# Performance work log

Hardware: AMD Instinct MI355X
Metric: run time of the kernel (lower is better)

The kernel has to match this reference:

```python
import jax, jax.numpy as jnp
import numpy as np

B, T, C, H = 8, 1024, 1024, 16
NEG = -1000000000.0
EPS = 1e-12


def setup_inputs() -> dict:
    key = jax.random.key(0)
    ks = jax.random.split(key, 12)
    s = 0.02  # keep pre-softmax logits in a sane range
    return {
        "x": jax.random.normal(ks[0], (B, T, C), jnp.float32),
        "mask": jax.random.randint(ks[1], (B, T), 0, 2, jnp.int32),
        "Wq": jax.random.normal(ks[2], (C, C), jnp.float32) * s,
        "bq": jax.random.normal(ks[3], (C,), jnp.float32) * s,
        "Wk": jax.random.normal(ks[4], (C, C), jnp.float32) * s,
        "bk": jax.random.normal(ks[5], (C,), jnp.float32) * s,
        "Wv": jax.random.normal(ks[6], (C, C), jnp.float32) * s,
        "bv": jax.random.normal(ks[7], (C,), jnp.float32) * s,
        "Wp": jax.random.normal(ks[8], (C, C), jnp.float32) * s,
        "bp": jax.random.normal(ks[9], (C,), jnp.float32) * s,
        "ln_w": jnp.ones((C,), jnp.float32),
        "ln_b": jnp.zeros((C,), jnp.float32),
    }


def reference(x, mask, Wq, bq, Wk, bk, Wv, bv, Wp, bp, ln_w, ln_b):
    Bx, Tx, Cx = x.shape
    hd = Cx // H
    # torch nn.Linear: y = x @ W.T + b
    def lin(inp, W, b):
        return inp @ W.T + b

    def split_heads(t):  # [B,T,C] -> [B,H,T,hd]
        return t.reshape(Bx, Tx, H, hd).transpose(0, 2, 1, 3)

    q = split_heads(lin(x, Wq, bq))
    k = split_heads(lin(x, Wk, bk))
    v = split_heads(lin(x, Wv, bv))

    att = jnp.einsum("bhqd,bhkd->bhqk", q, k) * (1.0 / jnp.sqrt(jnp.float32(hd)))
    # mask [B,T] masks key positions; broadcast to [B,1,1,T]
    att = jnp.where(mask[:, None, None, :] == 0, NEG, att)
    # stable softmax (manual max-subtract, matching original)
    att = jax.nn.softmax(att, axis=-1)
    # dropout prob 0.0 -> identity (eval-mode faithful)
    y = jnp.einsum("bhqk,bhkd->bhqd", att, v)
    y = y.transpose(0, 2, 1, 3).reshape(Bx, Tx, Cx)
    y = lin(y, Wp, bp)
    # residual + LayerNorm(eps=1e-12)
    z = y + x
    mu = jnp.mean(z, axis=-1, keepdims=True)
    var = jnp.mean(jnp.square(z - mu), axis=-1, keepdims=True)
    out = (z - mu) * jax.lax.rsqrt(var + EPS) * ln_w + ln_b
    return out
```

## Files before the change

kernel.cpp:

```cpp
#include <hip/hip_runtime.h>
#include <stdint.h>

#define B_ 8
#define T_ 1024
#define C_ 1024
#define H_ 16
#define HD 64
#define M_TOT (B_ * T_)

using f32x4 = __attribute__((ext_vector_type(4))) float;
using s16x8 = __attribute__((ext_vector_type(8))) short;
using i32x4 = __attribute__((ext_vector_type(4))) int;

__device__ __forceinline__ unsigned short f2bf(float f) {
  unsigned int u = __builtin_bit_cast(unsigned int, f);
  unsigned int r = (u + 0x7fffu + ((u >> 16) & 1u)) >> 16;
  return (unsigned short)r;
}

__device__ __forceinline__ void gload_lds16(const void* g, void* l) {
  __builtin_amdgcn_global_load_lds(
      (const __attribute__((address_space(1))) unsigned int*)g,
      (__attribute__((address_space(3))) unsigned int*)l, 16, 0, 0);
}

__global__ __launch_bounds__(256) void k_convert(
    const float* __restrict__ x, const float* __restrict__ wq,
    const float* __restrict__ wk, const float* __restrict__ wv,
    const float* __restrict__ wp, const float* __restrict__ bq,
    const float* __restrict__ bk, const float* __restrict__ bv,
    const int* __restrict__ maskp, unsigned short* __restrict__ xb,
    unsigned short* __restrict__ wqkv, unsigned short* __restrict__ wpb,
    float* __restrict__ bias_cat, unsigned int* __restrict__ mpair) {
  const long n_x = (long)M_TOT * C_;
  const long W_ELT = (long)C_ * C_;
  const long total4 = (n_x + 4 * W_ELT) >> 2;
  for (long i4 = (long)blockIdx.x * blockDim.x + threadIdx.x; i4 < total4;
       i4 += (long)gridDim.x * blockDim.x) {
    long i = i4 << 2;
    const float* src;
    unsigned short* dst;
    if (i < n_x) {
      src = x + i;
      dst = xb + i;
    } else {
      long off = i - n_x;
      int which = (int)(off >> 20);
      long wo = off & (W_ELT - 1);
      if (which < 3) {
        src = (which == 0 ? wq : which == 1 ? wk : wv) + wo;
        dst = wqkv + which * W_ELT + wo;
      } else {
        src = wp + wo;
        dst = wpb + wo;
      }
    }
    float4 v = *(const float4*)src;
    ushort4 u;
    u.x = f2bf(v.x); u.y = f2bf(v.y); u.z = f2bf(v.z); u.w = f2bf(v.w);
    *(ushort4*)dst = u;
  }
  int t = blockIdx.x * blockDim.x + threadIdx.x;
  if (t < 3 * C_) {
    float v = t < C_ ? bq[t] : (t < 2 * C_ ? bk[t - C_] : bv[t - 2 * C_]);
    bias_cat[t] = v;
  }
  if (t < B_ * T_ / 2) {
    const int* mr = maskp + t * 2;
    mpair[t] = (mr[0] ? 0xFFFFu : 0u) | (mr[1] ? 0xFFFF0000u : 0u);
  }
}

#define BM 128
#define BN 128
#define BK 32

template <int EPI>
__global__ __launch_bounds__(256, 2) void k_gemm(
    const unsigned short* __restrict__ A, const unsigned short* __restrict__ Bm,
    const float* __restrict__ bias, unsigned short* __restrict__ q_ws,
    unsigned short* __restrict__ k_ws, unsigned short* __restrict__ vt_ws,
    const float* __restrict__ xres, float* __restrict__ zout) {
  __shared__ unsigned short Al[2][BM * BK];
  __shared__ unsigned short Bl[2][BN * BK];
  const int tid = threadIdx.x, lane = tid & 63, w = tid >> 6;
  const int lc = lane & 15, lr = lane >> 4;
  const int GX = (EPI == 0) ? 24 : 8;
  const int NWG = GX * 64;
  int flat = blockIdx.y * GX + blockIdx.x;
  int swz = (flat & 7) * (NWG / 8) + (flat >> 3);
  const int m0 = (swz / GX) * BM, n0 = (swz % GX) * BN;
  const int wr = w >> 1, wc = w & 1;
  const char* Ab = (const char*)A;
  const char* Bb = (const char*)Bm;

  f32x4 acc[4][4] = {};

  auto stage = [&](int buf, int k0) {
#pragma unroll
    for (int it = 0; it < 2; ++it) {
      int f = it * 4096 + tid * 16;
      int row = f >> 6, colb = f & 63;
      gload_lds16(Ab + (long)(m0 + row) * (C_ * 2) + k0 * 2 + colb,
                  (char*)Al[buf] + it * 4096 + w * 1024);
      gload_lds16(Bb + (long)(n0 + row) * (C_ * 2) + k0 * 2 + colb,
                  (char*)Bl[buf] + it * 4096 + w * 1024);
    }
  };

  stage(0, 0);
  __syncthreads();
  int cur = 0;
  for (int k0 = 0; k0 < C_; k0 += BK) {
    if (k0 + BK < C_) stage(cur ^ 1, k0 + BK);
    s16x8 af[4], bfr[4];
#pragma unroll
    for (int mf = 0; mf < 4; ++mf)
      af[mf] = *(const s16x8*)&Al[cur][(wr * 64 + mf * 16 + lc) * BK + lr * 8];
#pragma unroll
    for (int nf = 0; nf < 4; ++nf)
      bfr[nf] = *(const s16x8*)&Bl[cur][(wc * 64 + nf * 16 + lc) * BK + lr * 8];
#pragma unroll
    for (int mf = 0; mf < 4; ++mf)
#pragma unroll
      for (int nf = 0; nf < 4; ++nf)
        acc[mf][nf] = __builtin_amdgcn_mfma_f32_16x16x32_bf16(af[mf], bfr[nf],
                                                              acc[mf][nf], 0, 0, 0);
    __syncthreads();
    cur ^= 1;
  }

  if (EPI == 0) {
#pragma unroll
    for (int mf = 0; mf < 4; ++mf)
#pragma unroll
      for (int nf = 0; nf < 4; ++nf) {
        int gn = n0 + wc * 64 + nf * 16 + lc;
        int which = gn >> 10, nn = gn & 1023;
        int hh = nn >> 6, dd = nn & 63;
        float bia = bias[gn];
        if (which == 2) {
          int gm = m0 + wr * 64 + mf * 16 + lr * 4;
          int bb = gm >> 10, tt = gm & 1023;
          ushort4 pk;
          pk.x = f2bf(acc[mf][nf][0] + bia);
          pk.y = f2bf(acc[mf][nf][1] + bia);
          pk.z = f2bf(acc[mf][nf][2] + bia);
          pk.w = f2bf(acc[mf][nf][3] + bia);
          *(ushort4*)&vt_ws[((long)(bb * H_ + hh) * HD + dd) * T_ + tt] = pk;
        } else {
          unsigned short* dst = (which == 0) ? q_ws : k_ws;
          float scl = (which == 0) ? 0.18033688011112042f : 1.0f;
#pragma unroll
          for (int i = 0; i < 4; ++i) {
            int gm = m0 + wr * 64 + mf * 16 + lr * 4 + i;
            int bb = gm >> 10, tt = gm & 1023;
            dst[((long)(bb * H_ + hh) * T_ + tt) * HD + dd] =
                f2bf((acc[mf][nf][i] + bia) * scl);
          }
        }
      }
  } else {
#pragma unroll
    for (int mf = 0; mf < 4; ++mf)
#pragma unroll
      for (int nf = 0; nf < 4; ++nf) {
        int gn = n0 + wc * 64 + nf * 16 + lc;
        float bia = bias[gn];
#pragma unroll
        for (int i = 0; i < 4; ++i) {
          int gm = m0 + wr * 64 + mf * 16 + lr * 4 + i;
          long idx = (long)gm * C_ + gn;
          zout[idx] = acc[mf][nf][i] + bia + xres[idx];
        }
      }
  }
}

__global__ __launch_bounds__(512, 4) void k_attn(
    const unsigned short* __restrict__ Qp, const unsigned short* __restrict__ Kp,
    const unsigned short* __restrict__ Vtp, const unsigned int* __restrict__ mpairp,
    unsigned short* __restrict__ Yp) {
  __shared__ unsigned short Kl[2][64 * 64];
  __shared__ unsigned short Vl[2][64 * 64];
  const int tid = threadIdx.x, lane = tid & 63, w = tid >> 6;
  const int bid = blockIdx.x;
  const int xcd = bid & 7, slot = bid >> 3;
  const int bh = xcd * 16 + (slot >> 3);
  const int qt = slot & 7;
  const int b = bh >> 4, h = bh & 15;
  const int lc = lane & 15, lr = lane >> 4;
  const int q0 = qt * 128 + w * 16;

  const unsigned short* qbase = Qp + ((long)bh * T_ + q0) * HD;
  s16x8 aq0 = *(const s16x8*)(qbase + lc * HD + lr * 8);
  s16x8 aq1 = *(const s16x8*)(qbase + lc * HD + 32 + lr * 8);

  s16x8 ones;
#pragma unroll
  for (int j = 0; j < 8; ++j) ones[j] = (short)0x3F80;

  f32x4 o[4] = {};
  f32x4 o_l = {};

  const char* kb_g = (const char*)(Kp + (long)bh * T_ * HD);
  const char* vb_g = (const char*)(Vtp + (long)bh * HD * T_);
  const unsigned int* mrow2 = mpairp + b * (T_ / 2);

  auto stage = [&](int buf, int kt) {
    int f = tid * 16;
    int row = f >> 7;
    int swz = (f & 127) ^ ((row & 7) << 4);
    gload_lds16(kb_g + (long)kt * 8192 + (f & ~127) + swz,
                (char*)Kl[buf] + w * 1024);
    gload_lds16(vb_g + (long)row * (T_ * 2) + kt * 128 + swz,
                (char*)Vl[buf] + w * 1024);
  };

  stage(0, 0);
  __syncthreads();

  const int s01 = lc + ((lane & 16) << 1);
  const int s23 = s01 + 16;
  const bool hi = (lane >= 32);

  int cur = 0;
  for (int kt = 0; kt < T_ / 64; ++kt) {
    if (kt + 1 < T_ / 64) stage(cur ^ 1, kt + 1);

    f32x4 s[4];
    const char* kl = (const char*)Kl[cur];
#pragma unroll
    for (int kf = 0; kf < 4; ++kf) {
      int key = kf * 16 + lc;
      s16x8 kb0 = *(const s16x8*)(kl + ((key * 128 + lr * 16) ^ ((key & 7) << 4)));
      s16x8 kb1 = *(const s16x8*)(kl + ((key * 128 + 64 + lr * 16) ^ ((key & 7) << 4)));
      f32x4 z = {};
      z = __builtin_amdgcn_mfma_f32_16x16x32_bf16(kb0, aq0, z, 0, 0, 0);
      z = __builtin_amdgcn_mfma_f32_16x16x32_bf16(kb1, aq1, z, 0, 0, 0);
      s[kf] = z;
    }

    unsigned int mw[4][2];
#pragma unroll
    for (int kf = 0; kf < 4; ++kf) {
      mw[kf][0] = mrow2[kt * 32 + kf * 8 + lr * 2];
      mw[kf][1] = mrow2[kt * 32 + kf * 8 + lr * 2 + 1];
    }

    unsigned int pk[4][2];
#pragma unroll
    for (int kf = 0; kf < 4; ++kf) {
      float p0 = __builtin_amdgcn_exp2f(s[kf][0]);
      float p1 = __builtin_amdgcn_exp2f(s[kf][1]);
      float p2 = __builtin_amdgcn_exp2f(s[kf][2]);
      float p3 = __builtin_amdgcn_exp2f(s[kf][3]);
      unsigned int u0 = __builtin_bit_cast(unsigned int, p0);
      unsigned int u1 = __builtin_bit_cast(unsigned int, p1);
      unsigned int u2 = __builtin_bit_cast(unsigned int, p2);
      unsigned int u3 = __builtin_bit_cast(unsigned int, p3);
      pk[kf][0] = ((u1 & 0xFFFF0000u) | (u0 >> 16)) & mw[kf][0];
      pk[kf][1] = ((u3 & 0xFFFF0000u) | (u2 >> 16)) & mw[kf][1];
    }

    s16x8 ap[2];
#pragma unroll
    for (int kc = 0; kc < 2; ++kc) {
      unsigned int A0 = pk[kc * 2][0], A1 = pk[kc * 2][1];
      unsigned int B0 = pk[kc * 2 + 1][0], B1 = pk[kc * 2 + 1][1];
      unsigned int w0a = __shfl((int)A0, s01, 64), w0b = __shfl((int)B0, s01, 64);
      unsigned int w1a = __shfl((int)A1, s01, 64), w1b = __shfl((int)B1, s01, 64);
      unsigned int w2a = __shfl((int)A0, s23, 64), w2b = __shfl((int)B0, s23, 64);
      unsigned int w3a = __shfl((int)A1, s23, 64), w3b = __shfl((int)B1, s23, 64);
      i32x4 wv;
      wv[0] = (int)(hi ? w0b : w0a);
      wv[1] = (int)(hi ? w1b : w1a);
      wv[2] = (int)(hi ? w2b : w2a);
      wv[3] = (int)(hi ? w3b : w3a);
      ap[kc] = __builtin_bit_cast(s16x8, wv);
    }

#pragma unroll
    for (int kc = 0; kc < 2; ++kc) {
      int koff = kc * 64 + lr * 16;
      o_l = __builtin_amdgcn_mfma_f32_16x16x32_bf16(ones, ap[kc], o_l, 0, 0, 0);
#pragma unroll
      for (int nf = 0; nf < 4; ++nf) {
        int drow = nf * 16 + lc;
        s16x8 vb = *(const s16x8*)((const char*)Vl[cur] +
                                   ((drow * 128 + koff) ^ ((drow & 7) << 4)));
        o[nf] = __builtin_amdgcn_mfma_f32_16x16x32_bf16(vb, ap[kc], o[nf], 0, 0, 0);
      }
    }
    __syncthreads();
    cur ^= 1;
  }

  float rl = 1.0f / o_l[0];
  unsigned short* yrow = Yp + ((long)(b * T_ + q0 + lc)) * C_ + h * 64;
#pragma unroll
  for (int nf = 0; nf < 4; ++nf) {
    ushort4 pw;
    pw.x = f2bf(o[nf][0] * rl);
    pw.y = f2bf(o[nf][1] * rl);
    pw.z = f2bf(o[nf][2] * rl);
    pw.w = f2bf(o[nf][3] * rl);
    *(ushort4*)(yrow + nf * 16 + lr * 4) = pw;
  }
}

__global__ __launch_bounds__(256) void k_ln(const float* __restrict__ z,
                                            const float* __restrict__ lw,
                                            const float* __restrict__ lb,
                                            float* __restrict__ out) {
  const int row = blockIdx.x;
  float4 v = ((const float4*)(z + (long)row * C_))[threadIdx.x];
  float s = v.x + v.y + v.z + v.w;
  float s2 = v.x * v.x + v.y * v.y + v.z * v.z + v.w * v.w;
#pragma unroll
  for (int d = 1; d < 64; d <<= 1) {
    s += __shfl_xor(s, d, 64);
    s2 += __shfl_xor(s2, d, 64);
  }
  __shared__ float rs[4], rq[4];
  int wv_ = threadIdx.x >> 6;
  if ((threadIdx.x & 63) == 0) { rs[wv_] = s; rq[wv_] = s2; }
  __syncthreads();
  s = rs[0] + rs[1] + rs[2] + rs[3];
  s2 = rq[0] + rq[1] + rq[2] + rq[3];
  float mu = s * (1.0f / C_);
  float var = s2 * (1.0f / C_) - mu * mu;
  float inv = rsqrtf(var + 1e-12f);
  float4 wv4 = ((const float4*)lw)[threadIdx.x];
  float4 bv4 = ((const float4*)lb)[threadIdx.x];
  float4 ov;
  ov.x = (v.x - mu) * inv * wv4.x + bv4.x;
  ov.y = (v.y - mu) * inv * wv4.y + bv4.y;
  ov.z = (v.z - mu) * inv * wv4.z + bv4.z;
  ov.w = (v.w - mu) * inv * wv4.w + bv4.w;
  ((float4*)(out + (long)row * C_))[threadIdx.x] = ov;
}

extern "C" void kernel_launch(void* const* d_in, const int* in_sizes, int n_in,
                              void* d_out, int out_size, void* d_ws,
                              size_t ws_size, hipStream_t stream) {
  const float* x = (const float*)d_in[0];
  const int* mask = (const int*)d_in[1];
  const float* Wq = (const float*)d_in[2];
  const float* bq = (const float*)d_in[3];
  const float* Wk = (const float*)d_in[4];
  const float* bk = (const float*)d_in[5];
  const float* Wv = (const float*)d_in[6];
  const float* bv = (const float*)d_in[7];
  const float* Wp = (const float*)d_in[8];
  const float* bp = (const float*)d_in[9];
  const float* lnw = (const float*)d_in[10];
  const float* lnb = (const float*)d_in[11];
  float* out = (float*)d_out;

  char* ws = (char*)d_ws;
  const size_t MB = 1024 * 1024;
  unsigned short* xb = (unsigned short*)(ws);
  unsigned short* q_ws = (unsigned short*)(ws + 16 * MB);
  unsigned short* k_ws = (unsigned short*)(ws + 32 * MB);
  unsigned short* vt_ws = (unsigned short*)(ws + 48 * MB);
  unsigned short* y_ws = (unsigned short*)(ws + 64 * MB);
  unsigned short* wqkv = (unsigned short*)(ws + 80 * MB);
  unsigned short* wpb = (unsigned short*)(ws + 86 * MB);
  float* bias_cat = (float*)(ws + 88 * MB);
  unsigned int* mpair = (unsigned int*)(ws + 88 * MB + 16384);
  float* z = (float*)(ws);

  k_convert<<<dim3(2048), dim3(256), 0, stream>>>(x, Wq, Wk, Wv, Wp, bq, bk, bv,
                                                  mask, xb, wqkv, wpb, bias_cat,
                                                  mpair);
  k_gemm<0><<<dim3(24, 64), dim3(256), 0, stream>>>(
      xb, wqkv, bias_cat, q_ws, k_ws, vt_ws, nullptr, nullptr);
  k_attn<<<dim3(1024), dim3(512), 0, stream>>>(q_ws, k_ws, vt_ws, mpair, y_ws);
  k_gemm<1><<<dim3(8, 64), dim3(256), 0, stream>>>(
      y_ws, wpb, bp, nullptr, nullptr, nullptr, x, z);
  k_ln<<<dim3(8192), dim3(256), 0, stream>>>(z, lnw, lnb, out);
}
```

Measured before the change: 197.4 us.

## Enlarge GEMM tiles to 256x128x64 with XOR-swizzled LDS and 8 waves

The projection GEMMs now use 512-thread blocks with a 256x128 output tile and BK=64, halving the grid in M. An XOR swizzle on the LDS layout is meant to avoid bank conflicts on the fragment reads. __syncthreads is replaced by an explicit vmcnt wait plus barrier. The goals are more operand reuse per global load and fewer loop iterations. In exchange, LDS use rises to 96KB per block, which could limit occupancy, and there are fewer blocks to spread across CUs.

```diff
diff --git a/kernel.cpp b/kernel.cpp
--- a/kernel.cpp
+++ b/kernel.cpp
@@ -71,76 +71,91 @@
   }
 }
 
-#define BM 128
-#define BN 128
-#define BK 32
-
 template <int EPI>
-__global__ __launch_bounds__(256, 2) void k_gemm(
+__global__ __launch_bounds__(512, 2) void k_gemm(
     const unsigned short* __restrict__ A, const unsigned short* __restrict__ Bm,
     const float* __restrict__ bias, unsigned short* __restrict__ q_ws,
     unsigned short* __restrict__ k_ws, unsigned short* __restrict__ vt_ws,
     const float* __restrict__ xres, float* __restrict__ zout) {
-  __shared__ unsigned short Al[2][BM * BK];
-  __shared__ unsigned short Bl[2][BN * BK];
+  __shared__ unsigned short Al[2][256 * 64];
+  __shared__ unsigned short Bl[2][128 * 64];
   const int tid = threadIdx.x, lane = tid & 63, w = tid >> 6;
   const int lc = lane & 15, lr = lane >> 4;
+  const int wm = w >> 1, wn = w & 1;
   const int GX = (EPI == 0) ? 24 : 8;
-  const int NWG = GX * 64;
+  const int NWG = GX * 32;
   int flat = blockIdx.y * GX + blockIdx.x;
   int swz = (flat & 7) * (NWG / 8) + (flat >> 3);
-  const int m0 = (swz / GX) * BM, n0 = (swz % GX) * BN;
-  const int wr = w >> 1, wc = w & 1;
+  const int m0 = (swz / GX) * 256, n0 = (swz % GX) * 128;
   const char* Ab = (const char*)A;
   const char* Bb = (const char*)Bm;
 
   f32x4 acc[4][4] = {};
 
-  auto stage = [&](int buf, int k0) {
-#pragma unroll
-    for (int it = 0; it < 2; ++it) {
-      int f = it * 4096 + tid * 16;
-      int row = f >> 6, colb = f & 63;
-      gload_lds16(Ab + (long)(m0 + row) * (C_ * 2) + k0 * 2 + colb,
-                  (char*)Al[buf] + it * 4096 + w * 1024);
-      gload_lds16(Bb + (long)(n0 + row) * (C_ * 2) + k0 * 2 + colb,
-                  (char*)Bl[buf] + it * 4096 + w * 1024);
+  auto stage = [&](int buf, int kt) {
+#pragma unroll
+    for (int i = 0; i < 4; ++i) {
+      int g = i * 512 + tid;
+      int row = g >> 3, gr = g & 7;
+      gload_lds16(Ab + (long)(m0 + row) * 2048 + kt * 128 + ((gr ^ (row & 7)) << 4),
+                  (char*)Al[buf] + (i * 512 + w * 64) * 16);
+    }
+#pragma unroll
+    for (int i = 0; i < 2; ++i) {
+      int g = i * 512 + tid;
+      int row = g >> 3, gr = g & 7;
+      gload_lds16(Bb + (long)(n0 + row) * 2048 + kt * 128 + ((gr ^ (row & 7)) << 4),
+                  (char*)Bl[buf] + (i * 512 + w * 64) * 16);
     }
   };
 
   stage(0, 0);
-  __syncthreads();
+  asm volatile("s_waitcnt vmcnt(0)" ::: "memory");
+  __builtin_amdgcn_s_barrier();
+  __builtin_amdgcn_sched_barrier(0);
+
   int cur = 0;
-  for (int k0 = 0; k0 < C_; k0 += BK) {
-    if (k0 + BK < C_) stage(cur ^ 1, k0 + BK);
-    s16x8 af[4], bfr[4];
+  for (int kt = 0; kt < C_ / 64; ++kt) {
+    if (kt + 1 < C_ / 64) stage(cur ^ 1, kt + 1);
+    const char* Ac = (const char*)Al[cur];
+    const char* Bc = (const char*)Bl[cur];
+#pragma unroll
+    for (int ks = 0; ks < 2; ++ks) {
+      s16x8 af[4], bfv[4];
+#pragma unroll
+      for (int mf = 0; mf < 4; ++mf) {
+        int ar = wm * 64 + mf * 16 + lc;
+        af[mf] = *(const s16x8*)(Ac + ar * 128 + (((ks * 4 + lr) ^ (ar & 7)) << 4));
+      }
+#pragma unroll
+      for (int nf = 0; nf < 4; ++nf) {
+        int br = wn * 64 + nf * 16 + lc;
+        bfv[nf] = *(const s16x8*)(Bc + br * 128 + (((ks * 4 + lr) ^ (br & 7)) << 4));
+      }
+#pragma unroll
+      for (int mf = 0; mf < 4; ++mf)
+#pragma unroll
+        for (int nf = 0; nf < 4; ++nf)
+          acc[mf][nf] = __builtin_amdgcn_mfma_f32_16x16x32_bf16(af[mf], bfv[nf],
+                                                                acc[mf][nf], 0, 0, 0);
+    }
+    asm volatile("s_waitcnt vmcnt(0)" ::: "memory");
+    __builtin_amdgcn_s_barrier();
+    __builtin_amdgcn_sched_barrier(0);
+    cur ^= 1;
+  }
+
+  if (EPI == 0) {
 #pragma unroll
     for (int mf = 0; mf < 4; ++mf)
-      af[mf] = *(const s16x8*)&Al[cur][(wr * 64 + mf * 16 + lc) * BK + lr * 8];
-#pragma unroll
-    for (int nf = 0; nf < 4; ++nf)
-      bfr[nf] = *(const s16x8*)&Bl[cur][(wc * 64 + nf * 16 + lc) * BK + lr * 8];
-#pragma unroll
-    for (int mf = 0; mf < 4; ++mf)
-#pragma unroll
-      for (int nf = 0; nf < 4; ++nf)
-        acc[mf][nf] = __builtin_amdgcn_mfma_f32_16x16x32_bf16(af[mf], bfr[nf],
-                                                              acc[mf][nf], 0, 0, 0);
-    __syncthreads();
-    cur ^= 1;
-  }
-
-  if (EPI == 0) {
-#pragma unroll
-    for (int mf = 0; mf < 4; ++mf)
 #pragma unroll
       for (int nf = 0; nf < 4; ++nf) {
-        int gn = n0 + wc * 64 + nf * 16 + lc;
+        int gn = n0 + wn * 64 + nf * 16 + lc;
         int which = gn >> 10, nn = gn & 1023;
         int hh = nn >> 6, dd = nn & 63;
         float bia = bias[gn];
         if (which == 2) {
-          int gm = m0 + wr * 64 + mf * 16 + lr * 4;
+          int gm = m0 + wm * 64 + mf * 16 + lr * 4;
           int bb = gm >> 10, tt = gm & 1023;
           ushort4 pk;
           pk.x = f2bf(acc[mf][nf][0] + bia);
@@ -153,7 +168,7 @@
           float scl = (which == 0) ? 0.18033688011112042f : 1.0f;
 #pragma unroll
           for (int i = 0; i < 4; ++i) {
-            int gm = m0 + wr * 64 + mf * 16 + lr * 4 + i;
+            int gm = m0 + wm * 64 + mf * 16 + lr * 4 + i;
             int bb = gm >> 10, tt = gm & 1023;
             dst[((long)(bb * H_ + hh) * T_ + tt) * HD + dd] =
                 f2bf((acc[mf][nf][i] + bia) * scl);
@@ -165,11 +180,11 @@
     for (int mf = 0; mf < 4; ++mf)
 #pragma unroll
       for (int nf = 0; nf < 4; ++nf) {
-        int gn = n0 + wc * 64 + nf * 16 + lc;
+        int gn = n0 + wn * 64 + nf * 16 + lc;
         float bia = bias[gn];
 #pragma unroll
         for (int i = 0; i < 4; ++i) {
-          int gm = m0 + wr * 64 + mf * 16 + lr * 4 + i;
+          int gm = m0 + wm * 64 + mf * 16 + lr * 4 + i;
           long idx = (long)gm * C_ + gn;
           zout[idx] = acc[mf][nf][i] + bia + xres[idx];
         }
@@ -374,10 +389,10 @@
   k_convert<<<dim3(2048), dim3(256), 0, stream>>>(x, Wq, Wk, Wv, Wp, bq, bk, bv,
                                                   mask, xb, wqkv, wpb, bias_cat,
                                                   mpair);
-  k_gemm<0><<<dim3(24, 64), dim3(256), 0, stream>>>(
+  k_gemm<0><<<dim3(24, 32), dim3(512), 0, stream>>>(
       xb, wqkv, bias_cat, q_ws, k_ws, vt_ws, nullptr, nullptr);
   k_attn<<<dim3(1024), dim3(512), 0, stream>>>(q_ws, k_ws, vt_ws, mpair, y_ws);
-  k_gemm<1><<<dim3(8, 64), dim3(256), 0, stream>>>(
+  k_gemm<1><<<dim3(8, 32), dim3(512), 0, stream>>>(
       y_ws, wpb, bp, nullptr, nullptr, nullptr, x, z);
   k_ln<<<dim3(8192), dim3(256), 0, stream>>>(z, lnw, lnb, out);
 }
```

Measured after the change: 190.0 us. 1.04x faster.
